# Kernel tuning notes

Hardware: AMD Instinct MI355X
Metric: run time of the kernel (lower is better)

Reference implementation:

```python
import jax, jax.numpy as jnp
import numpy as np

N = 100000        # nodes
E = 3200000       # edges (avg degree 32)
F_IN = 128        # input_dim
H = 64            # hidden_dim


def setup_inputs() -> dict:
    key = jax.random.key(0)
    ks = jax.random.split(key, 8)
    x = jax.random.normal(ks[0], (N, F_IN), dtype=jnp.float32)
    edge_index = jax.random.randint(ks[1], (2, E), 0, N, dtype=jnp.int64)
    # Glorot-ish init for GCNConv weights, zero bias (PyG default)
    def glorot(k, fan_in, fan_out):
        s = jnp.sqrt(6.0 / (fan_in + fan_out))
        return jax.random.uniform(k, (fan_in, fan_out), jnp.float32, -s, s)
    return {
        "x": x,
        "edge_index": edge_index,
        "W1": glorot(ks[2], F_IN, H), "b1": jnp.zeros((H,), jnp.float32),
        "W2": glorot(ks[3], H, H),    "b2": jnp.zeros((H,), jnp.float32),
        "W3": glorot(ks[4], H, H),    "b3": jnp.zeros((H,), jnp.float32),
    }


def _gcn_prep(edge_index):
    # add self-loops, compute symmetric normalization D^-1/2 (A+I) D^-1/2
    loop = jnp.arange(N, dtype=edge_index.dtype)
    src = jnp.concatenate([edge_index[0], loop])  # message sources
    dst = jnp.concatenate([edge_index[1], loop])  # aggregation targets
    deg = jax.ops.segment_sum(jnp.ones_like(dst, dtype=jnp.float32), dst, num_segments=N)
    dis = jnp.where(deg > 0, jax.lax.rsqrt(jnp.maximum(deg, 1.0)), 0.0)
    norm = dis[src] * dis[dst]  # [E+N]
    return src, dst, norm


def _gcn_conv(x, W, b, src, dst, norm):
    h = x @ W                                  # [N, H]
    msg = h[src] * norm[:, None]               # gather + scale, [E+N, H]
    out = jax.ops.segment_sum(msg, dst, num_segments=N)
    return out + b


def reference(x, edge_index, W1, b1, W2, b2, W3, b3):
    # GAEEncoder forward (eval mode: dropout p=0.2 is identity)
    src, dst, norm = _gcn_prep(edge_index)
    x = jax.nn.relu(_gcn_conv(x, W1, b1, src, dst, norm))
    x = jax.nn.relu(_gcn_conv(x, W2, b2, src, dst, norm))
    return _gcn_conv(x, W3, b3, src, dst, norm)
```

## Files before the change

### kernel.cpp

```cpp
#include <hip/hip_runtime.h>
#include <cstdint>

#define HDIM 64
#define BKT 98
#define BSHIFT 10
#define BCAP 36864
#define ECHUNK 4096

__device__ __forceinline__ float bflo(unsigned u) { return __uint_as_float(u << 16); }
__device__ __forceinline__ float bfhi(unsigned u) { return __uint_as_float(u & 0xffff0000u); }
__device__ __forceinline__ unsigned f2bf(float x) {
    unsigned b = __float_as_uint(x);
    return (b + 0x7fffu + ((b >> 16) & 1u)) >> 16;
}

__device__ __forceinline__ int edge_val(const void* ei, int is64, long long idx) {
    if (is64) return (int)((const long long*)ei)[idx];
    return ((const int*)ei)[idx];
}

__global__ __launch_bounds__(1024) void k_bucket(const unsigned* ei32, int* tails,
                                                 unsigned* packed, int E) {
    __shared__ int wcnt[4][16][BKT];
    __shared__ int wpre[4][16][BKT];
    __shared__ int gbase[BKT];
    __shared__ int is64_s;
    int tid = threadIdx.x;
    int lane = tid & 63, wid = tid >> 6;
    for (int i = tid; i < 4 * 16 * BKT; i += 1024) ((int*)wcnt)[i] = 0;
    if (tid == 0) is64_s = 1;
    __syncthreads();
    if (tid < 128 && ei32[2 * tid + 1] != 0u) is64_s = 0;
    __syncthreads();
    int is64 = is64_s;
    const void* ei = ei32;
    int b[4]; unsigned val[4]; int rank[4];
    int e0 = blockIdx.x * ECHUNK;
    unsigned long long below = (lane == 0) ? 0ull : ((~0ull) >> (64 - lane));
#pragma unroll
    for (int r = 0; r < 4; r++) {
        int e = e0 + r * 1024 + tid;
        b[r] = -1; val[r] = 0;
        if (e < E) {
            int d = edge_val(ei, is64, (long long)E + e);
            int s = edge_val(ei, is64, (long long)e);
            b[r] = d >> BSHIFT;
            val[r] = ((unsigned)(d & 1023) << 17) | (unsigned)s;
        }
        unsigned long long m = ~0ull;
#pragma unroll
        for (int bit = 0; bit < 7; bit++) {
            unsigned long long bb = __ballot(((unsigned)b[r] >> bit) & 1);
            m &= ((((unsigned)b[r] >> bit) & 1) ? bb : ~bb);
        }
        rank[r] = __popcll(m & below);
        if (b[r] >= 0 && rank[r] == 0) wcnt[r][wid][b[r]] = __popcll(m);
    }
    __syncthreads();
    if (tid < BKT) {
        int tot = 0;
#pragma unroll
        for (int r = 0; r < 4; r++)
#pragma unroll
            for (int w = 0; w < 16; w++) {
                wpre[r][w][tid] = tot;
                tot += wcnt[r][w][tid];
            }
        gbase[tid] = (tot > 0) ? atomicAdd(&tails[tid], tot) : 0;
    }
    __syncthreads();
#pragma unroll
    for (int r = 0; r < 4; r++) {
        if (b[r] >= 0) {
            int pos = gbase[b[r]] + wpre[r][wid][b[r]] + rank[r];
            if (pos < BCAP) packed[(size_t)b[r] * BCAP + pos] = val[r];
        }
    }
}

__global__ __launch_bounds__(1024) void k_build(const unsigned* packed, const int* tails,
                                                int* rowptr, float* dis, int* col, int N_) {
    __shared__ int cnt[1024];
    __shared__ int pfx[1024];
    __shared__ int fill[1024];
    __shared__ int rb_s;
    int b = blockIdx.x, tid = threadIdx.x;
    int v0 = (tid < BKT) ? min(tails[tid], BCAP) : 0;
    if (tid < 128) pfx[tid] = v0;
    __syncthreads();
    for (int off = 1; off < 128; off <<= 1) {
        int u = (tid >= off && tid < 128) ? pfx[tid - off] : 0;
        __syncthreads();
        if (tid < 128) pfx[tid] += u;
        __syncthreads();
    }
    if (tid == b) rb_s = pfx[tid] - v0;
    if (b == 0 && tid == BKT - 1) rowptr[N_] = pfx[BKT - 1];
    __syncthreads();
    int rowbase = rb_s;
    int nb_ = min(tails[b], BCAP);
    const unsigned* pb = packed + (size_t)b * BCAP;
    cnt[tid] = 0; fill[tid] = 0;
    __syncthreads();
    for (int s = tid; s < nb_; s += 1024)
        atomicAdd(&cnt[pb[s] >> 17], 1);
    __syncthreads();
    int v = cnt[tid];
    pfx[tid] = v;
    __syncthreads();
    for (int off = 1; off < 1024; off <<= 1) {
        int t = (tid >= off) ? pfx[tid - off] : 0;
        __syncthreads();
        pfx[tid] += t;
        __syncthreads();
    }
    int excl = pfx[tid] - v;
    int node = (b << BSHIFT) + tid;
    if (node < N_) {
        rowptr[node] = rowbase + excl;
        dis[node] = rsqrtf((float)(v + 1));
    }
    cnt[tid] = rowbase + excl;
    __syncthreads();
    for (int s = tid; s < nb_; s += 1024) {
        unsigned vv = pb[s];
        int dl = vv >> 17;
        int pos = cnt[dl] + atomicAdd(&fill[dl], 1);
        col[pos] = (int)(vv & 131071u);
    }
}

template <int K>
__device__ __forceinline__ int wswz(int lane, int k4) {
    if (K == 128) return k4 ^ (lane & 31);
    return ((k4 ^ (lane & 15)) + ((lane >> 4) << 2)) & 15;
}

template <int K, bool IN_BF16>
__global__ __launch_bounds__(256) void k_gemm_scale(const void* __restrict__ inp,
                                                    const float* __restrict__ W,
                                                    const float* __restrict__ dis,
                                                    unsigned* __restrict__ g2, int n) {
    constexpr int ROWS = (K == 128) ? 32 : 64;
    __shared__ float wt[64 * K];
    __shared__ float xs[ROWS * K];
    __shared__ float dsh[ROWS];
    int tid = threadIdx.x;
    for (int i = tid; i < K * 64; i += 256) {
        int k = i >> 6, f = i & 63;
        int k4 = k >> 2, j = k & 3;
        wt[f * K + (wswz<K>(f, k4) << 2) + j] = W[i];
    }
    int row0 = blockIdx.x * ROWS;
    int nrow = min(ROWS, n - row0);
    if (IN_BF16) {
        const unsigned* src = (const unsigned*)inp + (size_t)row0 * (K / 2);
        int nw = nrow * (K / 2);
        for (int i = tid; i < nw; i += 256) {
            unsigned u = src[i];
            xs[2 * i] = bflo(u);
            xs[2 * i + 1] = bfhi(u);
        }
    } else {
        const float4* src4 = (const float4*)((const float*)inp + (size_t)row0 * K);
        int nf4 = nrow * (K / 4);
        float4* xs4 = (float4*)xs;
        for (int i = tid; i < nf4; i += 256) xs4[i] = src4[i];
    }
    if (tid < nrow) dsh[tid] = dis[row0 + tid];
    __syncthreads();
    int lane = tid & 63, wid = tid >> 6;
    const float* wtl = wt + lane * K;
    constexpr int RW = ROWS / 4;
    for (int q = 0; q < RW; q += 4) {
        int rq = wid * RW + q;
        const float* x0 = xs + (size_t)(rq + 0) * K;
        const float* x1 = xs + (size_t)(rq + 1) * K;
        const float* x2 = xs + (size_t)(rq + 2) * K;
        const float* x3 = xs + (size_t)(rq + 3) * K;
        float a0 = 0.f, a1 = 0.f, a2 = 0.f, a3 = 0.f;
#pragma unroll 4
        for (int k4 = 0; k4 < K / 4; k4++) {
            float4 wv = *(const float4*)(wtl + (wswz<K>(lane, k4) << 2));
            float4 v0 = *(const float4*)(x0 + k4 * 4);
            float4 v1 = *(const float4*)(x1 + k4 * 4);
            float4 v2 = *(const float4*)(x2 + k4 * 4);
            float4 v3 = *(const float4*)(x3 + k4 * 4);
            a0 = fmaf(v0.x, wv.x, a0); a0 = fmaf(v0.y, wv.y, a0);
            a0 = fmaf(v0.z, wv.z, a0); a0 = fmaf(v0.w, wv.w, a0);
            a1 = fmaf(v1.x, wv.x, a1); a1 = fmaf(v1.y, wv.y, a1);
            a1 = fmaf(v1.z, wv.z, a1); a1 = fmaf(v1.w, wv.w, a1);
            a2 = fmaf(v2.x, wv.x, a2); a2 = fmaf(v2.y, wv.y, a2);
            a2 = fmaf(v2.z, wv.z, a2); a2 = fmaf(v2.w, wv.w, a2);
            a3 = fmaf(v3.x, wv.x, a3); a3 = fmaf(v3.y, wv.y, a3);
            a3 = fmaf(v3.z, wv.z, a3); a3 = fmaf(v3.w, wv.w, a3);
        }
        int gr = row0 + rq;
        bool wr = ((lane & 1) == 0);
        int wi = lane >> 1;
#pragma unroll
        for (int i = 0; i < 4; i++) {
            float a = (i == 0) ? a0 : (i == 1) ? a1 : (i == 2) ? a2 : a3;
            float v = a * dsh[rq + i];
            float p = __shfl_xor(v, 1);
            if (wr && gr + i < n)
                g2[(size_t)(gr + i) * 32 + wi] = f2bf(v) | (f2bf(p) << 16);
        }
    }
}

template <bool RELU, bool OUT32>
__global__ __launch_bounds__(256) void k_aggregate(const unsigned* __restrict__ g2,
                                                   const int* __restrict__ rowptr,
                                                   const int* __restrict__ col,
                                                   const float* __restrict__ dis,
                                                   const float* __restrict__ bias,
                                                   void* __restrict__ outp, int n) {
    int lane = threadIdx.x & 63;
    int wid = threadIdx.x >> 6;
    int li = lane & 15;
    int q = lane >> 4;
    int node = blockIdx.x * 4 + wid;
    if (node >= n) return;
    const uint2* g2v = (const uint2*)g2;
    float s0 = 0.f, s1 = 0.f, s2 = 0.f, s3 = 0.f;
    if (q == 0) {
        uint2 u = g2v[(size_t)node * 16 + li];
        s0 = bflo(u.x); s1 = bfhi(u.x); s2 = bflo(u.y); s3 = bfhi(u.y);
    }
    int e = rowptr[node], end = rowptr[node + 1];
    for (; e + 31 < end; e += 32) {
        int c0 = col[e + q],      c1 = col[e + 4 + q],  c2 = col[e + 8 + q],  c3 = col[e + 12 + q];
        int c4 = col[e + 16 + q], c5 = col[e + 20 + q], c6 = col[e + 24 + q], c7 = col[e + 28 + q];
        uint2 u0 = g2v[(size_t)c0 * 16 + li];
        uint2 u1 = g2v[(size_t)c1 * 16 + li];
        uint2 u2 = g2v[(size_t)c2 * 16 + li];
        uint2 u3 = g2v[(size_t)c3 * 16 + li];
        uint2 u4 = g2v[(size_t)c4 * 16 + li];
        uint2 u5 = g2v[(size_t)c5 * 16 + li];
        uint2 u6 = g2v[(size_t)c6 * 16 + li];
        uint2 u7 = g2v[(size_t)c7 * 16 + li];
        s0 += ((bflo(u0.x) + bflo(u1.x)) + (bflo(u2.x) + bflo(u3.x)))
            + ((bflo(u4.x) + bflo(u5.x)) + (bflo(u6.x) + bflo(u7.x)));
        s1 += ((bfhi(u0.x) + bfhi(u1.x)) + (bfhi(u2.x) + bfhi(u3.x)))
            + ((bfhi(u4.x) + bfhi(u5.x)) + (bfhi(u6.x) + bfhi(u7.x)));
        s2 += ((bflo(u0.y) + bflo(u1.y)) + (bflo(u2.y) + bflo(u3.y)))
            + ((bflo(u4.y) + bflo(u5.y)) + (bflo(u6.y) + bflo(u7.y)));
        s3 += ((bfhi(u0.y) + bfhi(u1.y)) + (bfhi(u2.y) + bfhi(u3.y)))
            + ((bfhi(u4.y) + bfhi(u5.y)) + (bfhi(u6.y) + bfhi(u7.y)));
    }
    for (; e + 15 < end; e += 16) {
        int c0 = col[e + q], c1 = col[e + 4 + q], c2 = col[e + 8 + q], c3 = col[e + 12 + q];
        uint2 u0 = g2v[(size_t)c0 * 16 + li];
        uint2 u1 = g2v[(size_t)c1 * 16 + li];
        uint2 u2 = g2v[(size_t)c2 * 16 + li];
        uint2 u3 = g2v[(size_t)c3 * 16 + li];
        s0 += ((bflo(u0.x) + bflo(u1.x)) + (bflo(u2.x) + bflo(u3.x)));
        s1 += ((bfhi(u0.x) + bfhi(u1.x)) + (bfhi(u2.x) + bfhi(u3.x)));
        s2 += ((bflo(u0.y) + bflo(u1.y)) + (bflo(u2.y) + bflo(u3.y)));
        s3 += ((bfhi(u0.y) + bfhi(u1.y)) + (bfhi(u2.y) + bfhi(u3.y)));
    }
    for (; e + 3 < end; e += 4) {
        int c = col[e + q];
        uint2 u = g2v[(size_t)c * 16 + li];
        s0 += bflo(u.x); s1 += bfhi(u.x); s2 += bflo(u.y); s3 += bfhi(u.y);
    }
    if (e < end) {
        int idx = e + q;
        bool valid = idx < end;
        int c = valid ? col[idx] : col[end - 1];
        uint2 u = g2v[(size_t)c * 16 + li];
        if (valid) { s0 += bflo(u.x); s1 += bfhi(u.x); s2 += bflo(u.y); s3 += bfhi(u.y); }
    }
    s0 += __shfl_xor(s0, 32); s0 += __shfl_xor(s0, 16);
    s1 += __shfl_xor(s1, 32); s1 += __shfl_xor(s1, 16);
    s2 += __shfl_xor(s2, 32); s2 += __shfl_xor(s2, 16);
    s3 += __shfl_xor(s3, 32); s3 += __shfl_xor(s3, 16);
    float4 b4 = ((const float4*)bias)[li];
    float dn = dis[node];
    float o0 = fmaf(dn, s0, b4.x);
    float o1 = fmaf(dn, s1, b4.y);
    float o2 = fmaf(dn, s2, b4.z);
    float o3 = fmaf(dn, s3, b4.w);
    if (RELU) {
        o0 = fmaxf(o0, 0.f); o1 = fmaxf(o1, 0.f);
        o2 = fmaxf(o2, 0.f); o3 = fmaxf(o3, 0.f);
    }
    if (q == 0) {
        if (OUT32) {
            ((float4*)outp)[(size_t)node * 16 + li] = make_float4(o0, o1, o2, o3);
        } else {
            uint2 st;
            st.x = f2bf(o0) | (f2bf(o1) << 16);
            st.y = f2bf(o2) | (f2bf(o3) << 16);
            ((uint2*)outp)[(size_t)node * 16 + li] = st;
        }
    }
}

extern "C" void kernel_launch(void* const* d_in, const int* in_sizes, int n_in,
                              void* d_out, int out_size, void* d_ws, size_t ws_size,
                              hipStream_t stream) {
    const float* x  = (const float*)d_in[0];
    const void*  ei = d_in[1];
    const float* W1 = (const float*)d_in[2];
    const float* b1 = (const float*)d_in[3];
    const float* W2 = (const float*)d_in[4];
    const float* b2 = (const float*)d_in[5];
    const float* W3 = (const float*)d_in[6];
    const float* b3 = (const float*)d_in[7];

    const int N = in_sizes[0] / 128;
    const int E = in_sizes[1] / 2;

    char* ws = (char*)d_ws;
    auto alloc = [&](size_t bytes) {
        char* p = ws;
        ws += ((bytes + 255) / 256) * 256;
        return p;
    };
    int*   tails  = (int*)alloc(BKT * 4);
    int*   rowptr = (int*)alloc((size_t)(N + 1) * 4);
    float* dis    = (float*)alloc((size_t)N * 4);
    int*   col    = (int*)alloc((size_t)E * 4);
    unsigned* bufA = (unsigned*)alloc((size_t)N * HDIM * 4);
    unsigned* bufB = (unsigned*)alloc((size_t)N * HDIM * 4);
    unsigned* packed = bufA;

    hipMemsetAsync(tails, 0, BKT * 4, stream);
    k_bucket<<<(E + ECHUNK - 1) / ECHUNK, 1024, 0, stream>>>((const unsigned*)ei, tails, packed, E);
    k_build<<<BKT, 1024, 0, stream>>>(packed, tails, rowptr, dis, col, N);

    const int aggGrid = (N + 3) / 4;

    k_gemm_scale<128, false><<<(N + 31) / 32, 256, 0, stream>>>(x, W1, dis, bufA, N);
    k_aggregate<true, false><<<aggGrid, 256, 0, stream>>>(bufA, rowptr, col, dis, b1, bufB, N);
    k_gemm_scale<64, true><<<(N + 63) / 64, 256, 0, stream>>>(bufB, W2, dis, bufA, N);
    k_aggregate<true, false><<<aggGrid, 256, 0, stream>>>(bufA, rowptr, col, dis, b2, bufB, N);
    k_gemm_scale<64, true><<<(N + 63) / 64, 256, 0, stream>>>(bufB, W3, dis, bufA, N);
    k_aggregate<false, true><<<aggGrid, 256, 0, stream>>>(bufA, rowptr, col, dis, b3, d_out, N);
}
```

Measured before the change: 414.0 us.

## Fuse next-layer GEMM into aggregation epilogue for layers two and three

The aggregation kernel for layers 1 and 2 now also multiplies the resulting per-node row by the next layer's weight matrix and the node's normalization factor, writing bf16 messages directly. This removes two standalone GEMM kernels and the bf16 round trip of the intermediate activations. In exchange, each aggregation block of only 4 nodes must load and swizzle the full 64x64 weight matrix into shared memory, which adds per-block overhead and LDS pressure across 25k blocks. It also changes rounding, since ReLU outputs are no longer stored in bf16 before the GEMM.

```diff
diff --git a/kernel.cpp b/kernel.cpp
--- a/kernel.cpp
+++ b/kernel.cpp
@@ -136,12 +136,11 @@
     return ((k4 ^ (lane & 15)) + ((lane >> 4) << 2)) & 15;
 }
 
-template <int K, bool IN_BF16>
-__global__ __launch_bounds__(256) void k_gemm_scale(const void* __restrict__ inp,
-                                                    const float* __restrict__ W,
-                                                    const float* __restrict__ dis,
-                                                    unsigned* __restrict__ g2, int n) {
-    constexpr int ROWS = (K == 128) ? 32 : 64;
+__global__ __launch_bounds__(256) void k_gemm128(const float* __restrict__ inp,
+                                                 const float* __restrict__ W,
+                                                 const float* __restrict__ dis,
+                                                 unsigned* __restrict__ g2, int n) {
+    constexpr int K = 128, ROWS = 32;
     __shared__ float wt[64 * K];
     __shared__ float xs[ROWS * K];
     __shared__ float dsh[ROWS];
@@ -153,20 +152,10 @@
     }
     int row0 = blockIdx.x * ROWS;
     int nrow = min(ROWS, n - row0);
-    if (IN_BF16) {
-        const unsigned* src = (const unsigned*)inp + (size_t)row0 * (K / 2);
-        int nw = nrow * (K / 2);
-        for (int i = tid; i < nw; i += 256) {
-            unsigned u = src[i];
-            xs[2 * i] = bflo(u);
-            xs[2 * i + 1] = bfhi(u);
-        }
-    } else {
-        const float4* src4 = (const float4*)((const float*)inp + (size_t)row0 * K);
-        int nf4 = nrow * (K / 4);
-        float4* xs4 = (float4*)xs;
-        for (int i = tid; i < nf4; i += 256) xs4[i] = src4[i];
-    }
+    const float4* src4 = (const float4*)(inp + (size_t)row0 * K);
+    int nf4 = nrow * (K / 4);
+    float4* xs4 = (float4*)xs;
+    for (int i = tid; i < nf4; i += 256) xs4[i] = src4[i];
     if (tid < nrow) dsh[tid] = dis[row0 + tid];
     __syncthreads();
     int lane = tid & 63, wid = tid >> 6;
@@ -209,20 +198,29 @@
     }
 }
 
-template <bool RELU, bool OUT32>
-__global__ __launch_bounds__(256) void k_aggregate(const unsigned* __restrict__ g2,
+__global__ __launch_bounds__(256) void k_agg_fused(const unsigned* __restrict__ g2in,
                                                    const int* __restrict__ rowptr,
                                                    const int* __restrict__ col,
                                                    const float* __restrict__ dis,
                                                    const float* __restrict__ bias,
-                                                   void* __restrict__ outp, int n) {
-    int lane = threadIdx.x & 63;
-    int wid = threadIdx.x >> 6;
+                                                   const float* __restrict__ Wn,
+                                                   unsigned* __restrict__ g2out, int n) {
+    __shared__ float wt[64 * 64];
+    __shared__ float xrow[4][64];
+    int tid = threadIdx.x;
+    for (int i = tid; i < 64 * 64; i += 256) {
+        int k = i >> 6, f = i & 63;
+        int k4 = k >> 2, j = k & 3;
+        wt[f * 64 + (wswz<64>(f, k4) << 2) + j] = Wn[i];
+    }
+    __syncthreads();
+    int lane = tid & 63;
+    int wave = tid >> 6;
     int li = lane & 15;
     int q = lane >> 4;
-    int node = blockIdx.x * 4 + wid;
+    int node = blockIdx.x * 4 + wave;
     if (node >= n) return;
-    const uint2* g2v = (const uint2*)g2;
+    const uint2* g2v = (const uint2*)g2in;
     float s0 = 0.f, s1 = 0.f, s2 = 0.f, s3 = 0.f;
     if (q == 0) {
         uint2 u = g2v[(size_t)node * 16 + li];
@@ -278,6 +276,96 @@
     s3 += __shfl_xor(s3, 32); s3 += __shfl_xor(s3, 16);
     float4 b4 = ((const float4*)bias)[li];
     float dn = dis[node];
+    float o0 = fmaxf(fmaf(dn, s0, b4.x), 0.f);
+    float o1 = fmaxf(fmaf(dn, s1, b4.y), 0.f);
+    float o2 = fmaxf(fmaf(dn, s2, b4.z), 0.f);
+    float o3 = fmaxf(fmaf(dn, s3, b4.w), 0.f);
+    if (q == 0) *(float4*)&xrow[wave][li * 4] = make_float4(o0, o1, o2, o3);
+    const float* wtl = wt + lane * 64;
+    const float* xr = xrow[wave];
+    float acc = 0.f;
+#pragma unroll 2
+    for (int k4 = 0; k4 < 16; k4++) {
+        float4 wv = *(const float4*)(wtl + (wswz<64>(lane, k4) << 2));
+        float4 xv = *(const float4*)(xr + k4 * 4);
+        acc = fmaf(xv.x, wv.x, acc); acc = fmaf(xv.y, wv.y, acc);
+        acc = fmaf(xv.z, wv.z, acc); acc = fmaf(xv.w, wv.w, acc);
+    }
+    float v = acc * dn;
+    float p = __shfl_xor(v, 1);
+    if ((lane & 1) == 0)
+        g2out[(size_t)node * 32 + (lane >> 1)] = f2bf(v) | (f2bf(p) << 16);
+}
+
+template <bool RELU, bool OUT32>
+__global__ __launch_bounds__(256) void k_aggregate(const unsigned* __restrict__ g2,
+                                                   const int* __restrict__ rowptr,
+                                                   const int* __restrict__ col,
+                                                   const float* __restrict__ dis,
+                                                   const float* __restrict__ bias,
+                                                   void* __restrict__ outp, int n) {
+    int lane = threadIdx.x & 63;
+    int wid = threadIdx.x >> 6;
+    int li = lane & 15;
+    int q = lane >> 4;
+    int node = blockIdx.x * 4 + wid;
+    if (node >= n) return;
+    const uint2* g2v = (const uint2*)g2;
+    float s0 = 0.f, s1 = 0.f, s2 = 0.f, s3 = 0.f;
+    if (q == 0) {
+        uint2 u = g2v[(size_t)node * 16 + li];
+        s0 = bflo(u.x); s1 = bfhi(u.x); s2 = bflo(u.y); s3 = bfhi(u.y);
+    }
+    int e = rowptr[node], end = rowptr[node + 1];
+    for (; e + 31 < end; e += 32) {
+        int c0 = col[e + q],      c1 = col[e + 4 + q],  c2 = col[e + 8 + q],  c3 = col[e + 12 + q];
+        int c4 = col[e + 16 + q], c5 = col[e + 20 + q], c6 = col[e + 24 + q], c7 = col[e + 28 + q];
+        uint2 u0 = g2v[(size_t)c0 * 16 + li];
+        uint2 u1 = g2v[(size_t)c1 * 16 + li];
+        uint2 u2 = g2v[(size_t)c2 * 16 + li];
+        uint2 u3 = g2v[(size_t)c3 * 16 + li];
+        uint2 u4 = g2v[(size_t)c4 * 16 + li];
+        uint2 u5 = g2v[(size_t)c5 * 16 + li];
+        uint2 u6 = g2v[(size_t)c6 * 16 + li];
+        uint2 u7 = g2v[(size_t)c7 * 16 + li];
+        s0 += ((bflo(u0.x) + bflo(u1.x)) + (bflo(u2.x) + bflo(u3.x)))
+            + ((bflo(u4.x) + bflo(u5.x)) + (bflo(u6.x) + bflo(u7.x)));
+        s1 += ((bfhi(u0.x) + bfhi(u1.x)) + (bfhi(u2.x) + bfhi(u3.x)))
+            + ((bfhi(u4.x) + bfhi(u5.x)) + (bfhi(u6.x) + bfhi(u7.x)));
+        s2 += ((bflo(u0.y) + bflo(u1.y)) + (bflo(u2.y) + bflo(u3.y)))
+            + ((bflo(u4.y) + bflo(u5.y)) + (bflo(u6.y) + bflo(u7.y)));
+        s3 += ((bfhi(u0.y) + bfhi(u1.y)) + (bfhi(u2.y) + bfhi(u3.y)))
+            + ((bfhi(u4.y) + bfhi(u5.y)) + (bfhi(u6.y) + bfhi(u7.y)));
+    }
+    for (; e + 15 < end; e += 16) {
+        int c0 = col[e + q], c1 = col[e + 4 + q], c2 = col[e + 8 + q], c3 = col[e + 12 + q];
+        uint2 u0 = g2v[(size_t)c0 * 16 + li];
+        uint2 u1 = g2v[(size_t)c1 * 16 + li];
+        uint2 u2 = g2v[(size_t)c2 * 16 + li];
+        uint2 u3 = g2v[(size_t)c3 * 16 + li];
+        s0 += ((bflo(u0.x) + bflo(u1.x)) + (bflo(u2.x) + bflo(u3.x)));
+        s1 += ((bfhi(u0.x) + bfhi(u1.x)) + (bfhi(u2.x) + bfhi(u3.x)));
+        s2 += ((bflo(u0.y) + bflo(u1.y)) + (bflo(u2.y) + bflo(u3.y)));
+        s3 += ((bfhi(u0.y) + bfhi(u1.y)) + (bfhi(u2.y) + bfhi(u3.y)));
+    }
+    for (; e + 3 < end; e += 4) {
+        int c = col[e + q];
+        uint2 u = g2v[(size_t)c * 16 + li];
+        s0 += bflo(u.x); s1 += bfhi(u.x); s2 += bflo(u.y); s3 += bfhi(u.y);
+    }
+    if (e < end) {
+        int idx = e + q;
+        bool valid = idx < end;
+        int c = valid ? col[idx] : col[end - 1];
+        uint2 u = g2v[(size_t)c * 16 + li];
+        if (valid) { s0 += bflo(u.x); s1 += bfhi(u.x); s2 += bflo(u.y); s3 += bfhi(u.y); }
+    }
+    s0 += __shfl_xor(s0, 32); s0 += __shfl_xor(s0, 16);
+    s1 += __shfl_xor(s1, 32); s1 += __shfl_xor(s1, 16);
+    s2 += __shfl_xor(s2, 32); s2 += __shfl_xor(s2, 16);
+    s3 += __shfl_xor(s3, 32); s3 += __shfl_xor(s3, 16);
+    float4 b4 = ((const float4*)bias)[li];
+    float dn = dis[node];
     float o0 = fmaf(dn, s0, b4.x);
     float o1 = fmaf(dn, s1, b4.y);
     float o2 = fmaf(dn, s2, b4.z);
@@ -333,10 +421,8 @@
 
     const int aggGrid = (N + 3) / 4;
 
-    k_gemm_scale<128, false><<<(N + 31) / 32, 256, 0, stream>>>(x, W1, dis, bufA, N);
-    k_aggregate<true, false><<<aggGrid, 256, 0, stream>>>(bufA, rowptr, col, dis, b1, bufB, N);
-    k_gemm_scale<64, true><<<(N + 63) / 64, 256, 0, stream>>>(bufB, W2, dis, bufA, N);
-    k_aggregate<true, false><<<aggGrid, 256, 0, stream>>>(bufA, rowptr, col, dis, b2, bufB, N);
-    k_gemm_scale<64, true><<<(N + 63) / 64, 256, 0, stream>>>(bufB, W3, dis, bufA, N);
+    k_gemm128<<<(N + 31) / 32, 256, 0, stream>>>(x, W1, dis, bufA, N);
+    k_agg_fused<<<aggGrid, 256, 0, stream>>>(bufA, rowptr, col, dis, b1, W2, bufB, N);
+    k_agg_fused<<<aggGrid, 256, 0, stream>>>(bufB, rowptr, col, dis, b2, W3, bufA, N);
     k_aggregate<false, true><<<aggGrid, 256, 0, stream>>>(bufA, rowptr, col, dis, b3, d_out, N);
 }
```

After: 401.4 us, median of 2. -3.1%, faster.
